# Performance work log

Measured on AMD Instinct MI355X. Metric: run time of the kernel, lower is better.

The kernel has to match this reference:

```python
import jax, jax.numpy as jnp
import numpy as np

N_NODES = 100000
N_EDGES = 1200000
D = 64
N_LAYERS = 3


def setup_inputs() -> dict:
    key = jax.random.key(0)
    k0, k1, k2, k3, k4 = jax.random.split(key, 5)
    x = jax.random.normal(k0, (N_NODES, D), dtype=jnp.float32)
    edge_index = jax.random.randint(k1, (2, N_EDGES), 0, N_NODES, dtype=jnp.int32)
    edge_weight = jax.random.uniform(k2, (N_EDGES,), dtype=jnp.float32)
    # stacked per-layer params: 3 layers of 64->64
    self_kernels = jax.random.normal(k3, (N_LAYERS, D, D), dtype=jnp.float32) * 0.1
    neighbor_kernels = jax.random.normal(k4, (N_LAYERS, D, D), dtype=jnp.float32) * 0.1
    biases = jnp.zeros((N_LAYERS, D), dtype=jnp.float32)
    return {"x": x, "edge_index": edge_index, "edge_weight": edge_weight,
            "self_kernels": self_kernels, "neighbor_kernels": neighbor_kernels,
            "biases": biases}


def _sage_layer(h, row, col, edge_weight, self_k, neigh_k, b):
    # gather source-node features per edge, weight them: [E, d]
    msg = h[col] * edge_weight[:, None]
    # sum-aggregate messages at target nodes: [N, d]
    agg = jax.ops.segment_sum(msg, row, num_segments=N_NODES)
    # concat=False -> self transform + neighbor transform added, then relu
    out = h @ self_k + agg @ neigh_k + b
    return jax.nn.relu(out)


def reference(x, edge_index, edge_weight, self_kernels, neighbor_kernels, biases):
    row, col = edge_index[0], edge_index[1]
    h = x
    for i in range(N_LAYERS):
        h = _sage_layer(h, row, col, edge_weight,
                        self_kernels[i], neighbor_kernels[i], biases[i])
    return h
```

## Files before the change

kernel.cpp:

```cpp
#include <hip/hip_runtime.h>

#define NN 100000
#define NE 1200000
#define DD 64
#define NTILES 3125
#define NBK 391
#define MLEN (NBK * 256)
#define EPB 4688

typedef unsigned int uint32;
typedef unsigned char uint8;
typedef unsigned short ushort16;
typedef __attribute__((ext_vector_type(8))) short short8;
typedef __attribute__((ext_vector_type(16))) float f32x16;

__device__ __forceinline__ ushort16 f2bf(float x) {
    uint32 u = __float_as_uint(x);
    u += 0x7FFFu + ((u >> 16) & 1u);
    return (ushort16)(u >> 16);
}
__device__ __forceinline__ float bflo(uint32 u) { return __uint_as_float(u << 16); }
__device__ __forceinline__ float bfhi(uint32 u) { return __uint_as_float(u & 0xFFFF0000u); }
__device__ __forceinline__ uint32 pack2(float a, float b) {
    return (uint32)f2bf(a) | ((uint32)f2bf(b) << 16);
}


__global__ __launch_bounds__(512)
void k_bcount(const int* __restrict__ row, int* __restrict__ M) {
    __shared__ int bins[NBK];
    for (int i = threadIdx.x; i < NBK; i += 512) bins[i] = 0;
    __syncthreads();
    int start = blockIdx.x * EPB;
    int end = min(start + EPB, NE);
    for (int e = start + (int)threadIdx.x; e < end; e += 512)
        atomicAdd(&bins[row[e] >> 8], 1);
    __syncthreads();
    for (int i = threadIdx.x; i < NBK; i += 512)
        M[i * 256 + blockIdx.x] = bins[i];
}

__global__ void k_scan1(const int* __restrict__ in, int* __restrict__ outx,
                        int* __restrict__ partials) {
    __shared__ int tmp[256];
    int t = threadIdx.x;
    int i = blockIdx.x * 256 + t;
    int v = (i < MLEN) ? in[i] : 0;
    tmp[t] = v;
    __syncthreads();
    #pragma unroll
    for (int off = 1; off < 256; off <<= 1) {
        int add = (t >= off) ? tmp[t - off] : 0;
        __syncthreads();
        tmp[t] += add;
        __syncthreads();
    }
    if (i < MLEN) outx[i] = tmp[t] - v;
    if (t == 255) partials[blockIdx.x] = tmp[255];
}

__global__ void k_scan2(int* __restrict__ partials) {
    __shared__ int tmp[512];
    int t = threadIdx.x;
    int v = (t < NBK) ? partials[t] : 0;
    tmp[t] = v;
    __syncthreads();
    #pragma unroll
    for (int off = 1; off < 512; off <<= 1) {
        int add = (t >= off) ? tmp[t - off] : 0;
        __syncthreads();
        tmp[t] += add;
        __syncthreads();
    }
    if (t < NBK) partials[t] = tmp[t] - v;
}

__global__ __launch_bounds__(512)
void k_bscatter(const int* __restrict__ row, const int* __restrict__ col,
                const float* __restrict__ ew, const int* __restrict__ Mscan,
                const int* __restrict__ partials,
                uint32* __restrict__ colw, uint8* __restrict__ rowlo) {
    __shared__ int cur[NBK];
    for (int i = threadIdx.x; i < NBK; i += 512)
        cur[i] = Mscan[i * 256 + blockIdx.x] + partials[i];
    __syncthreads();
    int start = blockIdx.x * EPB;
    int end = min(start + EPB, NE);
    for (int e = start + (int)threadIdx.x; e < end; e += 512) {
        int r = row[e];
        int wq = (int)(ew[e] * 32767.0f + 0.5f);
        wq = (wq > 32767) ? 32767 : wq;
        int p = atomicAdd(&cur[r >> 8], 1);
        colw[p]  = ((uint32)col[e] << 15) | (uint32)wq;
        rowlo[p] = (uint8)(r & 255);
    }
}

__global__ __launch_bounds__(256)
void k_build(const int* __restrict__ Mscan, const int* __restrict__ partials,
             const uint32* __restrict__ colw, const uint8* __restrict__ rowlo,
             uint32* __restrict__ edges, int* __restrict__ offsets) {
    __shared__ int bins[256];
    __shared__ int tmp[256];
    __shared__ int cur[256];
    int b = blockIdx.x;
    int t = threadIdx.x;
    int bstart = Mscan[b * 256] + partials[b];
    int bend   = (b == NBK - 1) ? NE : Mscan[(b + 1) * 256] + partials[b + 1];
    bins[t] = 0;
    __syncthreads();
    for (int p = bstart + t; p < bend; p += 256)
        atomicAdd(&bins[rowlo[p]], 1);
    __syncthreads();
    int v = bins[t];
    tmp[t] = v;
    __syncthreads();
    #pragma unroll
    for (int off = 1; off < 256; off <<= 1) {
        int add = (t >= off) ? tmp[t - off] : 0;
        __syncthreads();
        tmp[t] += add;
        __syncthreads();
    }
    int base = bstart + (tmp[t] - v);
    cur[t] = base;
    int rowid = b * 256 + t;
    if (rowid < NN) offsets[rowid] = base;
    if (b == 0 && t == 0) offsets[NN] = NE;
    __syncthreads();
    for (int p = bstart + t; p < bend; p += 256) {
        uint32 cw = colw[p];
        int dst = atomicAdd(&cur[rowlo[p]], 1);
        edges[dst] = cw;
    }
}


__global__ void k_packW(const float* __restrict__ selfk,
                        const float* __restrict__ neighk,
                        short8* __restrict__ wpack) {
    int tid = blockIdx.x * 256 + threadIdx.x;
    if (tid >= 3 * 16 * 64) return;
    int lane  = tid & 63;
    int frag  = (tid >> 6) & 15;
    int layer = tid >> 10;
    int g = frag >> 3;
    int t = (frag >> 2) & 1;
    int s = frag & 3;
    const float* W = (g ? neighk : selfk) + layer * 4096;
    int n = t * 32 + (lane & 31);
    int k0 = s * 16 + (lane >> 5) * 8;
    short8 v;
    #pragma unroll
    for (int j = 0; j < 8; j++) v[j] = (short)f2bf(W[(k0 + j) * 64 + n]);
    wpack[tid] = v;
}


__global__ __launch_bounds__(256)
void gemm_mfma(const float* __restrict__ hf_, ushort16* __restrict__ hs,
               ushort16* __restrict__ y,
               const short8* __restrict__ wpack,
               const float* __restrict__ bias) {
    int lane  = threadIdx.x & 63;
    int wave  = threadIdx.x >> 6;
    int wid   = blockIdx.x * 4 + wave;
    int nwv   = gridDim.x * 4;
    int mrow  = lane & 31;
    int khalf = lane >> 5;
    int t     = wid & 1;

    short8 Wf[2][4];
    #pragma unroll
    for (int g = 0; g < 2; g++)
        #pragma unroll
        for (int s = 0; s < 4; s++)
            Wf[g][s] = wpack[(((g * 2 + t) * 4) + s) * 64 + lane];

    float bval = bias[t * 32 + mrow];

    for (int tile = wid >> 1; tile < NTILES; tile += nwv >> 1) {
        int n0 = tile * 32;
        const float* hf = hf_ + (n0 + mrow) * 64 + khalf * 8;
        short8 A[4];
        #pragma unroll
        for (int s = 0; s < 4; s++) {
            short8 a;
            #pragma unroll
            for (int j = 0; j < 8; j++) a[j] = (short)f2bf(hf[s * 16 + j]);
            A[s] = a;
        }

        f32x16 acc0, acc1;
        #pragma unroll
        for (int r = 0; r < 16; r++) { acc0[r] = 0.f; acc1[r] = 0.f; }

        #pragma unroll
        for (int s = 0; s < 4; s++) {
            acc0 = __builtin_amdgcn_mfma_f32_32x32x16_bf16(A[s], Wf[0][s], acc0, 0, 0, 0);
            acc1 = __builtin_amdgcn_mfma_f32_32x32x16_bf16(A[s], Wf[1][s], acc1, 0, 0, 0);
        }

        int colbase = t * 32 + mrow;
        #pragma unroll
        for (int r = 0; r < 16; r++) {
            int rw = (r & 3) + 8 * (r >> 2) + 4 * khalf;
            int n = n0 + rw;
            hs[n * DD + colbase] = f2bf(acc0[r] + bval);
            y [n * DD + colbase] = f2bf(acc1[r]);
        }
    }
}


__global__ __launch_bounds__(256)
void agg_gemm(const uint2* __restrict__ hs2, const uint2* __restrict__ y2,
              ushort16* __restrict__ hs_out, ushort16* __restrict__ y_out,
              const int* __restrict__ offsets, const uint32* __restrict__ edges,
              const short8* __restrict__ wpack, const float* __restrict__ bias) {
    __shared__ uint32 sh[32 * 36];
    int lane = threadIdx.x & 63;
    int wave = threadIdx.x >> 6;
    int g  = lane >> 4;
    int fl = lane & 15;
    int n0 = blockIdx.x * 32;

    #pragma unroll
    for (int q = 0; q < 2; q++) {
        int lrow = wave * 8 + q * 4 + g;
        int n = n0 + lrow;
        uint2 hv = hs2[n * 16 + fl];
        float a0 = bflo(hv.x), a1 = bfhi(hv.x), a2 = bflo(hv.y), a3 = bfhi(hv.y);
        int s = offsets[n], e = offsets[n + 1];
        #pragma unroll 4
        for (int j = s; j < e; j++) {
            uint32 ed = edges[j];
            int c = (int)(ed >> 15);
            float w = (float)(ed & 32767u) * (1.0f / 32767.0f);
            uint2 yv = y2[c * 16 + fl];
            a0 = fmaf(bflo(yv.x), w, a0);
            a1 = fmaf(bfhi(yv.x), w, a1);
            a2 = fmaf(bflo(yv.y), w, a2);
            a3 = fmaf(bfhi(yv.y), w, a3);
        }
        sh[lrow * 36 + fl * 2]     = pack2(fmaxf(a0, 0.f), fmaxf(a1, 0.f));
        sh[lrow * 36 + fl * 2 + 1] = pack2(fmaxf(a2, 0.f), fmaxf(a3, 0.f));
    }
    __syncthreads();

    int mrow  = lane & 31;
    int khalf = lane >> 5;
    int gsel  = wave >> 1;
    int t     = wave & 1;

    short8 Wf[4];
    #pragma unroll
    for (int s = 0; s < 4; s++)
        Wf[s] = wpack[(((gsel * 2 + t) * 4) + s) * 64 + lane];

    short8 A[4];
    #pragma unroll
    for (int s = 0; s < 4; s++)
        A[s] = *(const short8*)&sh[mrow * 36 + s * 8 + khalf * 4];

    f32x16 acc;
    #pragma unroll
    for (int r = 0; r < 16; r++) acc[r] = 0.f;
    #pragma unroll
    for (int s = 0; s < 4; s++)
        acc = __builtin_amdgcn_mfma_f32_32x32x16_bf16(A[s], Wf[s], acc, 0, 0, 0);

    float bval = gsel ? 0.f : bias[t * 32 + mrow];
    ushort16* dst = gsel ? y_out : hs_out;
    int colbase = t * 32 + mrow;
    #pragma unroll
    for (int r = 0; r < 16; r++) {
        int rw = (r & 3) + 8 * (r >> 2) + 4 * khalf;
        int n = n0 + rw;
        dst[n * DD + colbase] = f2bf(acc[r] + bval);
    }
}


__global__ __launch_bounds__(256)
void agg_final(const uint2* __restrict__ hs2, const uint2* __restrict__ y2,
               float4* __restrict__ out, const int* __restrict__ offsets,
               const uint32* __restrict__ edges) {
    int lane = threadIdx.x & 63;
    int wave = threadIdx.x >> 6;
    int g  = lane >> 4;
    int fl = lane & 15;
    int n = (blockIdx.x * 4 + wave) * 4 + g;

    uint2 hv = hs2[n * 16 + fl];
    float a0 = bflo(hv.x), a1 = bfhi(hv.x), a2 = bflo(hv.y), a3 = bfhi(hv.y);

    int s = offsets[n], e = offsets[n + 1];
    #pragma unroll 4
    for (int j = s; j < e; j++) {
        uint32 ed = edges[j];
        int c = (int)(ed >> 15);
        float w = (float)(ed & 32767u) * (1.0f / 32767.0f);
        uint2 yv = y2[c * 16 + fl];
        a0 = fmaf(bflo(yv.x), w, a0);
        a1 = fmaf(bfhi(yv.x), w, a1);
        a2 = fmaf(bflo(yv.y), w, a2);
        a3 = fmaf(bfhi(yv.y), w, a3);
    }
    out[n * 16 + fl] = make_float4(fmaxf(a0, 0.f), fmaxf(a1, 0.f),
                                   fmaxf(a2, 0.f), fmaxf(a3, 0.f));
}


extern "C" void kernel_launch(void* const* d_in, const int* in_sizes, int n_in,
                              void* d_out, int out_size, void* d_ws, size_t ws_size,
                              hipStream_t stream) {
    const float* x      = (const float*)d_in[0];
    const int*   ei     = (const int*)d_in[1];
    const float* ew     = (const float*)d_in[2];
    const float* selfk  = (const float*)d_in[3];
    const float* neighk = (const float*)d_in[4];
    const float* biases = (const float*)d_in[5];
    float* out = (float*)d_out;

    char* w = (char*)d_ws;
    ushort16* hsA   = (ushort16*)w; w += (size_t)NN * DD * sizeof(ushort16);
    ushort16* yA    = (ushort16*)w; w += (size_t)NN * DD * sizeof(ushort16);
    ushort16* hsB   = (ushort16*)w; w += (size_t)NN * DD * sizeof(ushort16);
    ushort16* yB    = (ushort16*)w; w += (size_t)NN * DD * sizeof(ushort16);
    uint32* edges   = (uint32*)w;   w += (size_t)NE * sizeof(uint32);
    uint32* colwB   = (uint32*)w;   w += (size_t)NE * sizeof(uint32);
    uint8*  rowlo   = (uint8*)w;    w += (size_t)NE * sizeof(uint8);
    w = (char*)(((size_t)w + 255) & ~(size_t)255);
    int*    M       = (int*)w;      w += (size_t)MLEN * sizeof(int);
    int*    Mscan   = (int*)w;      w += (size_t)MLEN * sizeof(int);
    int*    offsets = (int*)w;      w += (size_t)(NN + 1) * sizeof(int);
    int*    partials= (int*)w;      w += 512 * sizeof(int);
    short8* wpack   = (short8*)w;   w += (size_t)3 * 16 * 64 * sizeof(short8);

    const int* row = ei;
    const int* col = ei + NE;

    k_packW   <<<12, 256, 0, stream>>>(selfk, neighk, wpack);
    k_bcount  <<<256, 512, 0, stream>>>(row, M);
    k_scan1   <<<NBK, 256, 0, stream>>>(M, Mscan, partials);
    k_scan2   <<<1, 512, 0, stream>>>(partials);
    k_bscatter<<<256, 512, 0, stream>>>(row, col, ew, Mscan, partials, colwB, rowlo);
    k_build   <<<NBK, 256, 0, stream>>>(Mscan, partials, colwB, rowlo, edges, offsets);

    gemm_mfma<<<782, 256, 0, stream>>>(x, hsA, yA, wpack, biases);
    agg_gemm <<<NTILES, 256, 0, stream>>>((const uint2*)hsA, (const uint2*)yA,
                                          hsB, yB, offsets, edges,
                                          wpack + 1024, biases + 64);
    agg_gemm <<<NTILES, 256, 0, stream>>>((const uint2*)hsB, (const uint2*)yB,
                                          hsA, yA, offsets, edges,
                                          wpack + 2048, biases + 128);
    agg_final<<<NN / 16, 256, 0, stream>>>((const uint2*)hsA, (const uint2*)yA,
                                           (float4*)out, offsets, edges);
}
```

Before: 232.5 us.

## Fuse CSR build and weight packing into one cooperative kernel with grid syncs

Merges the six preprocessing kernels (weight pack, bucket count, two scans, bucket scatter, per-bucket build) into one cooperative launch that uses grid.sync between phases. Scans now use wave shuffle primitives in place of the shared-memory Hillis-Steele loops. The aim is to remove several kernel launch gaps and the serial single-block scan. In exchange, grid-wide barriers add cost, and the cooperative launch requires all 391 blocks of 512 threads to be resident at once.

```diff
diff --git a/kernel.cpp b/kernel.cpp
--- a/kernel.cpp
+++ b/kernel.cpp
@@ -1,11 +1,13 @@
 #include <hip/hip_runtime.h>
+#include <hip/hip_cooperative_groups.h>
+
+namespace cg = cooperative_groups;
 
 #define NN 100000
 #define NE 1200000
 #define DD 64
 #define NTILES 3125
 #define NBK 391
-#define MLEN (NBK * 256)
 #define EPB 4688
 
 typedef unsigned int uint32;
@@ -24,136 +26,130 @@
 __device__ __forceinline__ uint32 pack2(float a, float b) {
     return (uint32)f2bf(a) | ((uint32)f2bf(b) << 16);
 }
+__device__ __forceinline__ int wave_incl_scan(int v) {
+    #pragma unroll
+    for (int d = 1; d < 64; d <<= 1) {
+        int u = __shfl_up(v, d);
+        if ((int)(threadIdx.x & 63) >= d) v += u;
+    }
+    return v;
+}
 
 
 __global__ __launch_bounds__(512)
-void k_bcount(const int* __restrict__ row, int* __restrict__ M) {
-    __shared__ int bins[NBK];
-    for (int i = threadIdx.x; i < NBK; i += 512) bins[i] = 0;
-    __syncthreads();
-    int start = blockIdx.x * EPB;
-    int end = min(start + EPB, NE);
-    for (int e = start + (int)threadIdx.x; e < end; e += 512)
-        atomicAdd(&bins[row[e] >> 8], 1);
-    __syncthreads();
-    for (int i = threadIdx.x; i < NBK; i += 512)
-        M[i * 256 + blockIdx.x] = bins[i];
-}
-
-__global__ void k_scan1(const int* __restrict__ in, int* __restrict__ outx,
-                        int* __restrict__ partials) {
-    __shared__ int tmp[256];
-    int t = threadIdx.x;
-    int i = blockIdx.x * 256 + t;
-    int v = (i < MLEN) ? in[i] : 0;
-    tmp[t] = v;
-    __syncthreads();
-    #pragma unroll
-    for (int off = 1; off < 256; off <<= 1) {
-        int add = (t >= off) ? tmp[t - off] : 0;
-        __syncthreads();
-        tmp[t] += add;
-        __syncthreads();
-    }
-    if (i < MLEN) outx[i] = tmp[t] - v;
-    if (t == 255) partials[blockIdx.x] = tmp[255];
-}
-
-__global__ void k_scan2(int* __restrict__ partials) {
-    __shared__ int tmp[512];
-    int t = threadIdx.x;
-    int v = (t < NBK) ? partials[t] : 0;
-    tmp[t] = v;
-    __syncthreads();
-    #pragma unroll
-    for (int off = 1; off < 512; off <<= 1) {
-        int add = (t >= off) ? tmp[t - off] : 0;
-        __syncthreads();
-        tmp[t] += add;
-        __syncthreads();
-    }
-    if (t < NBK) partials[t] = tmp[t] - v;
-}
-
-__global__ __launch_bounds__(512)
-void k_bscatter(const int* __restrict__ row, const int* __restrict__ col,
-                const float* __restrict__ ew, const int* __restrict__ Mscan,
-                const int* __restrict__ partials,
-                uint32* __restrict__ colw, uint8* __restrict__ rowlo) {
-    __shared__ int cur[NBK];
-    for (int i = threadIdx.x; i < NBK; i += 512)
-        cur[i] = Mscan[i * 256 + blockIdx.x] + partials[i];
-    __syncthreads();
-    int start = blockIdx.x * EPB;
-    int end = min(start + EPB, NE);
-    for (int e = start + (int)threadIdx.x; e < end; e += 512) {
-        int r = row[e];
-        int wq = (int)(ew[e] * 32767.0f + 0.5f);
-        wq = (wq > 32767) ? 32767 : wq;
-        int p = atomicAdd(&cur[r >> 8], 1);
-        colw[p]  = ((uint32)col[e] << 15) | (uint32)wq;
-        rowlo[p] = (uint8)(r & 255);
-    }
-}
-
-__global__ __launch_bounds__(256)
-void k_build(const int* __restrict__ Mscan, const int* __restrict__ partials,
-             const uint32* __restrict__ colw, const uint8* __restrict__ rowlo,
-             uint32* __restrict__ edges, int* __restrict__ offsets) {
-    __shared__ int bins[256];
-    __shared__ int tmp[256];
-    __shared__ int cur[256];
+void k_csr(const int* __restrict__ row, const int* __restrict__ col,
+           const float* __restrict__ ew,
+           const float* __restrict__ selfk, const float* __restrict__ neighk,
+           short8* __restrict__ wpack,
+           int* __restrict__ M, int* __restrict__ totals, int* __restrict__ Mscan,
+           uint32* __restrict__ colw, uint8* __restrict__ rowlo,
+           uint32* __restrict__ edges, int* __restrict__ offsets) {
+    cg::grid_group grid = cg::this_grid();
+    __shared__ int sBins[NBK];
+    __shared__ int sPart[NBK];
+    __shared__ int sB2[256];
     int b = blockIdx.x;
     int t = threadIdx.x;
-    int bstart = Mscan[b * 256] + partials[b];
-    int bend   = (b == NBK - 1) ? NE : Mscan[(b + 1) * 256] + partials[b + 1];
-    bins[t] = 0;
-    __syncthreads();
-    for (int p = bstart + t; p < bend; p += 256)
-        atomicAdd(&bins[rowlo[p]], 1);
-    __syncthreads();
-    int v = bins[t];
-    tmp[t] = v;
-    __syncthreads();
-    #pragma unroll
-    for (int off = 1; off < 256; off <<= 1) {
-        int add = (t >= off) ? tmp[t - off] : 0;
+    int lane = t & 63;
+
+    {
+        int tid = b * 512 + t;
+        if (tid < 3 * 16 * 64) {
+            int wl    = tid & 63;
+            int frag  = (tid >> 6) & 15;
+            int layer = tid >> 10;
+            int g = frag >> 3, th = (frag >> 2) & 1, s = frag & 3;
+            const float* W = (g ? neighk : selfk) + layer * 4096;
+            int n = th * 32 + (wl & 31);
+            int k0 = s * 16 + (wl >> 5) * 8;
+            short8 v;
+            #pragma unroll
+            for (int j = 0; j < 8; j++) v[j] = (short)f2bf(W[(k0 + j) * 64 + n]);
+            wpack[tid] = v;
+        }
+    }
+
+    for (int i = t; i < NBK; i += 512) sBins[i] = 0;
+    __syncthreads();
+    if (b < 256) {
+        int start = b * EPB, end = min(start + EPB, NE);
+        for (int e = start + t; e < end; e += 512)
+            atomicAdd(&sBins[row[e] >> 8], 1);
         __syncthreads();
-        tmp[t] += add;
+        for (int i = t; i < NBK; i += 512) M[i * 256 + b] = sBins[i];
+    }
+    grid.sync();
+
+    if (t < 64) {
+        int carry = 0;
+        #pragma unroll
+        for (int c = 0; c < 4; c++) {
+            int v = M[b * 256 + c * 64 + lane];
+            int incl = wave_incl_scan(v);
+            Mscan[b * 256 + c * 64 + lane] = carry + incl - v;
+            carry += __shfl(incl, 63);
+        }
+        if (lane == 0) totals[b] = carry;
+    }
+    grid.sync();
+
+    if (t < 64) {
+        int carry = 0;
+        #pragma unroll
+        for (int c = 0; c < 7; c++) {
+            int idx = c * 64 + lane;
+            int v = (idx < NBK) ? totals[idx] : 0;
+            int incl = wave_incl_scan(v);
+            if (idx < NBK) sPart[idx] = carry + incl - v;
+            carry += __shfl(incl, 63);
+        }
+    }
+    __syncthreads();
+    if (b < 256) {
+        for (int i = t; i < NBK; i += 512) sBins[i] = Mscan[i * 256 + b] + sPart[i];
         __syncthreads();
-    }
-    int base = bstart + (tmp[t] - v);
-    cur[t] = base;
-    int rowid = b * 256 + t;
-    if (rowid < NN) offsets[rowid] = base;
+        int start = b * EPB, end = min(start + EPB, NE);
+        for (int e = start + t; e < end; e += 512) {
+            int r = row[e];
+            int wq = (int)(ew[e] * 32767.0f + 0.5f);
+            wq = (wq > 32767) ? 32767 : wq;
+            int p = atomicAdd(&sBins[r >> 8], 1);
+            colw[p]  = ((uint32)col[e] << 15) | (uint32)wq;
+            rowlo[p] = (uint8)(r & 255);
+        }
+    }
+    grid.sync();
+
+    int bstart = sPart[b];
+    int bend   = bstart + totals[b];
+    if (t < 256) sBins[t] = 0;
+    __syncthreads();
+    for (int p = bstart + t; p < bend; p += 512)
+        atomicAdd(&sBins[rowlo[p]], 1);
+    __syncthreads();
+    if (t < 64) {
+        int carry = 0;
+        #pragma unroll
+        for (int c = 0; c < 4; c++) {
+            int v = sBins[c * 64 + lane];
+            int incl = wave_incl_scan(v);
+            sB2[c * 64 + lane] = bstart + carry + incl - v;
+            carry += __shfl(incl, 63);
+        }
+    }
+    __syncthreads();
+    if (t < 256) {
+        int rowid = b * 256 + t;
+        if (rowid < NN) offsets[rowid] = sB2[t];
+        sBins[t] = sB2[t];
+    }
     if (b == 0 && t == 0) offsets[NN] = NE;
     __syncthreads();
-    for (int p = bstart + t; p < bend; p += 256) {
+    for (int p = bstart + t; p < bend; p += 512) {
         uint32 cw = colw[p];
-        int dst = atomicAdd(&cur[rowlo[p]], 1);
+        int dst = atomicAdd(&sBins[rowlo[p]], 1);
         edges[dst] = cw;
     }
-}
-
-
-__global__ void k_packW(const float* __restrict__ selfk,
-                        const float* __restrict__ neighk,
-                        short8* __restrict__ wpack) {
-    int tid = blockIdx.x * 256 + threadIdx.x;
-    if (tid >= 3 * 16 * 64) return;
-    int lane  = tid & 63;
-    int frag  = (tid >> 6) & 15;
-    int layer = tid >> 10;
-    int g = frag >> 3;
-    int t = (frag >> 2) & 1;
-    int s = frag & 3;
-    const float* W = (g ? neighk : selfk) + layer * 4096;
-    int n = t * 32 + (lane & 31);
-    int k0 = s * 16 + (lane >> 5) * 8;
-    short8 v;
-    #pragma unroll
-    for (int j = 0; j < 8; j++) v[j] = (short)f2bf(W[(k0 + j) * 64 + n]);
-    wpack[tid] = v;
 }
 
 
@@ -332,21 +328,21 @@
     uint32* colwB   = (uint32*)w;   w += (size_t)NE * sizeof(uint32);
     uint8*  rowlo   = (uint8*)w;    w += (size_t)NE * sizeof(uint8);
     w = (char*)(((size_t)w + 255) & ~(size_t)255);
-    int*    M       = (int*)w;      w += (size_t)MLEN * sizeof(int);
-    int*    Mscan   = (int*)w;      w += (size_t)MLEN * sizeof(int);
+    int*    M       = (int*)w;      w += (size_t)NBK * 256 * sizeof(int);
+    int*    Mscan   = (int*)w;      w += (size_t)NBK * 256 * sizeof(int);
     int*    offsets = (int*)w;      w += (size_t)(NN + 1) * sizeof(int);
-    int*    partials= (int*)w;      w += 512 * sizeof(int);
+    int*    totals  = (int*)w;      w += 512 * sizeof(int);
     short8* wpack   = (short8*)w;   w += (size_t)3 * 16 * 64 * sizeof(short8);
 
     const int* row = ei;
     const int* col = ei + NE;
 
-    k_packW   <<<12, 256, 0, stream>>>(selfk, neighk, wpack);
-    k_bcount  <<<256, 512, 0, stream>>>(row, M);
-    k_scan1   <<<NBK, 256, 0, stream>>>(M, Mscan, partials);
-    k_scan2   <<<1, 512, 0, stream>>>(partials);
-    k_bscatter<<<256, 512, 0, stream>>>(row, col, ew, Mscan, partials, colwB, rowlo);
-    k_build   <<<NBK, 256, 0, stream>>>(Mscan, partials, colwB, rowlo, edges, offsets);
+    void* args[] = {(void*)&row, (void*)&col, (void*)&ew,
+                    (void*)&selfk, (void*)&neighk, (void*)&wpack,
+                    (void*)&M, (void*)&totals, (void*)&Mscan,
+                    (void*)&colwB, (void*)&rowlo, (void*)&edges, (void*)&offsets};
+    hipLaunchCooperativeKernel((const void*)k_csr, dim3(NBK), dim3(512),
+                               args, 0, stream);
 
     gemm_mfma<<<782, 256, 0, stream>>>(x, hsA, yA, wpack, biases);
     agg_gemm <<<NTILES, 256, 0, stream>>>((const uint2*)hsA, (const uint2*)yA,
```

Result: slower. 392.3 us (+68.7%).

## Fuse first-layer GEMM with bucket count and pack weights on the fly

Applied to the files above, without the earlier changes.

The separate weight-packing kernel, the bucket-count kernel and the first-layer GEMM are merged into one launch. Blocks 0-255 do the edge bucket histogram and the remaining blocks run the layer-0 MFMA GEMM. Every agg_gemm block now converts its weight fragments from fp32 straight into bf16 fragments instead of reading a prepacked buffer. This removes two kernel launches and lets independent work overlap, but adds strided fp32 weight loads and conversion work in every agg_gemm block and wave.

```diff
diff --git a/kernel.cpp b/kernel.cpp
--- a/kernel.cpp
+++ b/kernel.cpp
@@ -7,6 +7,7 @@
 #define NBK 391
 #define MLEN (NBK * 256)
 #define EPB 4688
+#define GEMM_BLOCKS 782
 
 typedef unsigned int uint32;
 typedef unsigned char uint8;
@@ -25,20 +26,82 @@
     return (uint32)f2bf(a) | ((uint32)f2bf(b) << 16);
 }
 
-
-__global__ __launch_bounds__(512)
-void k_bcount(const int* __restrict__ row, int* __restrict__ M) {
+__device__ __forceinline__ short8 packWfrag(const float* __restrict__ W,
+                                            int s, int t, int mrow, int khalf) {
+    short8 v;
+    const float* p = W + (s * 16 + khalf * 8) * 64 + t * 32 + mrow;
+    #pragma unroll
+    for (int j = 0; j < 8; j++) v[j] = (short)f2bf(p[j * 64]);
+    return v;
+}
+
+
+__global__ __launch_bounds__(256)
+void k_gemm_bcount(const float* __restrict__ x,
+                   ushort16* __restrict__ hs, ushort16* __restrict__ y,
+                   const float* __restrict__ selfk, const float* __restrict__ neighk,
+                   const float* __restrict__ bias,
+                   const int* __restrict__ row, int* __restrict__ M) {
     __shared__ int bins[NBK];
-    for (int i = threadIdx.x; i < NBK; i += 512) bins[i] = 0;
-    __syncthreads();
-    int start = blockIdx.x * EPB;
-    int end = min(start + EPB, NE);
-    for (int e = start + (int)threadIdx.x; e < end; e += 512)
-        atomicAdd(&bins[row[e] >> 8], 1);
-    __syncthreads();
-    for (int i = threadIdx.x; i < NBK; i += 512)
-        M[i * 256 + blockIdx.x] = bins[i];
-}
+    int t = threadIdx.x;
+    if (blockIdx.x < 256) {
+        int b = blockIdx.x;
+        for (int i = t; i < NBK; i += 256) bins[i] = 0;
+        __syncthreads();
+        int start = b * EPB, end = min(start + EPB, NE);
+        for (int e = start + t; e < end; e += 256)
+            atomicAdd(&bins[row[e] >> 8], 1);
+        __syncthreads();
+        for (int i = t; i < NBK; i += 256) M[i * 256 + b] = bins[i];
+        return;
+    }
+    int lane  = t & 63;
+    int wave  = t >> 6;
+    int wid   = (blockIdx.x - 256) * 4 + wave;
+    int mrow  = lane & 31;
+    int khalf = lane >> 5;
+    int th    = wid & 1;
+
+    short8 Wf[2][4];
+    #pragma unroll
+    for (int s = 0; s < 4; s++) {
+        Wf[0][s] = packWfrag(selfk,  s, th, mrow, khalf);
+        Wf[1][s] = packWfrag(neighk, s, th, mrow, khalf);
+    }
+    float bval = bias[th * 32 + mrow];
+
+    for (int tile = wid >> 1; tile < NTILES; tile += (GEMM_BLOCKS * 4) >> 1) {
+        int n0 = tile * 32;
+        const float* hf = x + (n0 + mrow) * 64 + khalf * 8;
+        short8 A[4];
+        #pragma unroll
+        for (int s = 0; s < 4; s++) {
+            short8 a;
+            #pragma unroll
+            for (int j = 0; j < 8; j++) a[j] = (short)f2bf(hf[s * 16 + j]);
+            A[s] = a;
+        }
+
+        f32x16 acc0, acc1;
+        #pragma unroll
+        for (int r = 0; r < 16; r++) { acc0[r] = 0.f; acc1[r] = 0.f; }
+        #pragma unroll
+        for (int s = 0; s < 4; s++) {
+            acc0 = __builtin_amdgcn_mfma_f32_32x32x16_bf16(A[s], Wf[0][s], acc0, 0, 0, 0);
+            acc1 = __builtin_amdgcn_mfma_f32_32x32x16_bf16(A[s], Wf[1][s], acc1, 0, 0, 0);
+        }
+
+        int colbase = th * 32 + mrow;
+        #pragma unroll
+        for (int r = 0; r < 16; r++) {
+            int rw = (r & 3) + 8 * (r >> 2) + 4 * khalf;
+            int n = n0 + rw;
+            hs[n * DD + colbase] = f2bf(acc0[r] + bval);
+            y [n * DD + colbase] = f2bf(acc1[r]);
+        }
+    }
+}
+
 
 __global__ void k_scan1(const int* __restrict__ in, int* __restrict__ outx,
                         int* __restrict__ partials) {
@@ -136,94 +199,27 @@
 }
 
 
-__global__ void k_packW(const float* __restrict__ selfk,
-                        const float* __restrict__ neighk,
-                        short8* __restrict__ wpack) {
-    int tid = blockIdx.x * 256 + threadIdx.x;
-    if (tid >= 3 * 16 * 64) return;
-    int lane  = tid & 63;
-    int frag  = (tid >> 6) & 15;
-    int layer = tid >> 10;
-    int g = frag >> 3;
-    int t = (frag >> 2) & 1;
-    int s = frag & 3;
-    const float* W = (g ? neighk : selfk) + layer * 4096;
-    int n = t * 32 + (lane & 31);
-    int k0 = s * 16 + (lane >> 5) * 8;
-    short8 v;
-    #pragma unroll
-    for (int j = 0; j < 8; j++) v[j] = (short)f2bf(W[(k0 + j) * 64 + n]);
-    wpack[tid] = v;
-}
-
-
-__global__ __launch_bounds__(256)
-void gemm_mfma(const float* __restrict__ hf_, ushort16* __restrict__ hs,
-               ushort16* __restrict__ y,
-               const short8* __restrict__ wpack,
-               const float* __restrict__ bias) {
-    int lane  = threadIdx.x & 63;
-    int wave  = threadIdx.x >> 6;
-    int wid   = blockIdx.x * 4 + wave;
-    int nwv   = gridDim.x * 4;
-    int mrow  = lane & 31;
-    int khalf = lane >> 5;
-    int t     = wid & 1;
-
-    short8 Wf[2][4];
-    #pragma unroll
-    for (int g = 0; g < 2; g++)
-        #pragma unroll
-        for (int s = 0; s < 4; s++)
-            Wf[g][s] = wpack[(((g * 2 + t) * 4) + s) * 64 + lane];
-
-    float bval = bias[t * 32 + mrow];
-
-    for (int tile = wid >> 1; tile < NTILES; tile += nwv >> 1) {
-        int n0 = tile * 32;
-        const float* hf = hf_ + (n0 + mrow) * 64 + khalf * 8;
-        short8 A[4];
-        #pragma unroll
-        for (int s = 0; s < 4; s++) {
-            short8 a;
-            #pragma unroll
-            for (int j = 0; j < 8; j++) a[j] = (short)f2bf(hf[s * 16 + j]);
-            A[s] = a;
-        }
-
-        f32x16 acc0, acc1;
-        #pragma unroll
-        for (int r = 0; r < 16; r++) { acc0[r] = 0.f; acc1[r] = 0.f; }
-
-        #pragma unroll
-        for (int s = 0; s < 4; s++) {
-            acc0 = __builtin_amdgcn_mfma_f32_32x32x16_bf16(A[s], Wf[0][s], acc0, 0, 0, 0);
-            acc1 = __builtin_amdgcn_mfma_f32_32x32x16_bf16(A[s], Wf[1][s], acc1, 0, 0, 0);
-        }
-
-        int colbase = t * 32 + mrow;
-        #pragma unroll
-        for (int r = 0; r < 16; r++) {
-            int rw = (r & 3) + 8 * (r >> 2) + 4 * khalf;
-            int n = n0 + rw;
-            hs[n * DD + colbase] = f2bf(acc0[r] + bval);
-            y [n * DD + colbase] = f2bf(acc1[r]);
-        }
-    }
-}
-
-
 __global__ __launch_bounds__(256)
 void agg_gemm(const uint2* __restrict__ hs2, const uint2* __restrict__ y2,
               ushort16* __restrict__ hs_out, ushort16* __restrict__ y_out,
               const int* __restrict__ offsets, const uint32* __restrict__ edges,
-              const short8* __restrict__ wpack, const float* __restrict__ bias) {
+              const float* __restrict__ selfk, const float* __restrict__ neighk,
+              const float* __restrict__ bias) {
     __shared__ uint32 sh[32 * 36];
     int lane = threadIdx.x & 63;
     int wave = threadIdx.x >> 6;
     int g  = lane >> 4;
     int fl = lane & 15;
     int n0 = blockIdx.x * 32;
+
+    int mrow  = lane & 31;
+    int khalf = lane >> 5;
+    int gsel  = wave >> 1;
+    int t     = wave & 1;
+    const float* W = gsel ? neighk : selfk;
+    short8 Wf[4];
+    #pragma unroll
+    for (int s = 0; s < 4; s++) Wf[s] = packWfrag(W, s, t, mrow, khalf);
 
     #pragma unroll
     for (int q = 0; q < 2; q++) {
@@ -248,16 +244,6 @@
     }
     __syncthreads();
 
-    int mrow  = lane & 31;
-    int khalf = lane >> 5;
-    int gsel  = wave >> 1;
-    int t     = wave & 1;
-
-    short8 Wf[4];
-    #pragma unroll
-    for (int s = 0; s < 4; s++)
-        Wf[s] = wpack[(((gsel * 2 + t) * 4) + s) * 64 + lane];
-
     short8 A[4];
     #pragma unroll
     for (int s = 0; s < 4; s++)
@@ -336,25 +322,23 @@
     int*    Mscan   = (int*)w;      w += (size_t)MLEN * sizeof(int);
     int*    offsets = (int*)w;      w += (size_t)(NN + 1) * sizeof(int);
     int*    partials= (int*)w;      w += 512 * sizeof(int);
-    short8* wpack   = (short8*)w;   w += (size_t)3 * 16 * 64 * sizeof(short8);
 
     const int* row = ei;
     const int* col = ei + NE;
 
-    k_packW   <<<12, 256, 0, stream>>>(selfk, neighk, wpack);
-    k_bcount  <<<256, 512, 0, stream>>>(row, M);
+    k_gemm_bcount<<<256 + GEMM_BLOCKS, 256, 0, stream>>>(x, hsA, yA, selfk, neighk,
+                                                         biases, row, M);
     k_scan1   <<<NBK, 256, 0, stream>>>(M, Mscan, partials);
     k_scan2   <<<1, 512, 0, stream>>>(partials);
     k_bscatter<<<256, 512, 0, stream>>>(row, col, ew, Mscan, partials, colwB, rowlo);
     k_build   <<<NBK, 256, 0, stream>>>(Mscan, partials, colwB, rowlo, edges, offsets);
 
-    gemm_mfma<<<782, 256, 0, stream>>>(x, hsA, yA, wpack, biases);
     agg_gemm <<<NTILES, 256, 0, stream>>>((const uint2*)hsA, (const uint2*)yA,
                                           hsB, yB, offsets, edges,
-                                          wpack + 1024, biases + 64);
+                                          selfk + 4096, neighk + 4096, biases + 64);
     agg_gemm <<<NTILES, 256, 0, stream>>>((const uint2*)hsB, (const uint2*)yB,
                                           hsA, yA, offsets, edges,
-                                          wpack + 2048, biases + 128);
+                                          selfk + 2 * 4096, neighk + 2 * 4096, biases + 128);
     agg_final<<<NN / 16, 256, 0, stream>>>((const uint2*)hsA, (const uint2*)yA,
                                            (float4*)out, offsets, edges);
 }
```

New measurement: 250.0 us. +7.5%, slower.
